# Kernel optimization log

Hardware: AMD Instinct MI355X
Metric: run time of the kernel (lower is better)

## Reference

```python
import jax, jax.numpy as jnp
import numpy as np

K, D = 1024, 256


def setup_inputs() -> dict:
    key = jax.random.key(0)
    k1, k2 = jax.random.split(key)
    z_e = jax.random.normal(k1, (32, D, 32, 32), dtype=jnp.float32)
    # torch init: uniform_(-1/K, 1/K)
    emb_weight = jax.random.uniform(k2, (K, D), minval=-1.0 / K, maxval=1.0 / K, dtype=jnp.float32)
    return {"z_e": z_e, "emb_weight": emb_weight}


def reference(z_e, emb_weight):
    B, C, W, H = z_e.shape
    # [B, W, H, C] -> flatten to [N, C]
    z = jnp.transpose(z_e, (0, 2, 3, 1))
    z_flat = z.reshape(-1, C)
    # squared euclidean distances; argmin is identical to argmin of cdist
    d2 = (
        jnp.sum(z_flat * z_flat, axis=1, keepdims=True)
        - 2.0 * (z_flat @ emb_weight.T)
        + jnp.sum(emb_weight * emb_weight, axis=1)
    )  # [N, K]
    indices = jnp.argmin(d2, axis=1)  # [N]
    z_q = emb_weight[indices].reshape(B, W, H, C)
    # straight-through: forward value equals z_q, gradient passes to z_e
    z_q_st = z + jax.lax.stop_gradient(z_q - z)
    z_q_out = jnp.transpose(z_q, (0, 3, 1, 2))
    z_q_st_out = jnp.transpose(z_q_st, (0, 3, 1, 2))
    return (z_q_st_out, z_q_out, indices.reshape(B, W * H))
```

## Files before the change

### kernel.cpp

```cpp
#include <hip/hip_runtime.h>
#include <cfloat>
#include <cstdint>

#define THRESH 1.25e-4f

typedef __attribute__((ext_vector_type(8))) _Float16 half8;
typedef __attribute__((ext_vector_type(8))) unsigned short upk8;
typedef __attribute__((ext_vector_type(4))) float facc4;

__device__ __forceinline__ unsigned short f2h(float x) {
  _Float16 h = (_Float16)x;
  return __builtin_bit_cast(unsigned short, h);
}


__global__ __launch_bounds__(256) void precompute_kernel(
    const float* __restrict__ emb, float* __restrict__ Csq,
    unsigned short* __restrict__ ehT, int* __restrict__ flagCount) {
  int blk = blockIdx.x, t = threadIdx.x;
  if (blk < 4) {
    int k = blk * 256 + t;
    const float4* e4 = (const float4*)(emb + ((size_t)k << 8));
    double acc = 0.0;
    for (int d4 = 0; d4 < 64; ++d4) {
      float4 e = e4[d4];
      acc += (double)(e.x * e.x) + (double)(e.y * e.y) +
             (double)(e.z * e.z) + (double)(e.w * e.w);
    }
    Csq[k] = (float)acc;
    if (blk == 0 && t == 0) *flagCount = 0;
  } else {
    int linear = (blk - 4) * 256 + t;
    int code = linear & 1023, kg = linear >> 10;
    const float* ep = emb + ((size_t)code << 8) + (kg << 3);
    float4 e0 = *(const float4*)ep;
    float4 e1 = *(const float4*)(ep + 4);
    upk8 pk;
    pk[0] = f2h(e0.x); pk[1] = f2h(e0.y); pk[2] = f2h(e0.z); pk[3] = f2h(e0.w);
    pk[4] = f2h(e1.x); pk[5] = f2h(e1.y); pk[6] = f2h(e1.z); pk[7] = f2h(e1.w);
    *(upk8*)(ehT + ((size_t)linear << 3)) = pk;
  }
}

__device__ __forceinline__ void stage_half(
    const unsigned short* __restrict__ ehT, char* buf, int h, int t) {
  int w6 = t & 0x1C0;
#pragma unroll
  for (int i = 0; i < 8; ++i) {
    int slot = (i << 9) + t;
    int kg = slot >> 7, cl = slot & 127;
    const unsigned short* g = ehT + (((size_t)(kg << 10) + (h << 7) + cl) << 3);
    char* lp = buf + (((i << 9) + w6) << 4);
    __builtin_amdgcn_global_load_lds(
        (const __attribute__((address_space(1))) unsigned int*)g,
        (__attribute__((address_space(3))) unsigned int*)lp, 16, 0, 0);
  }
}

__global__ __launch_bounds__(512) __attribute__((amdgpu_waves_per_eu(2, 2)))
void phase1_kernel(
    const float* __restrict__ z, const unsigned short* __restrict__ ehT,
    const float* __restrict__ Csq, float* __restrict__ A,
    int* __restrict__ idxbuf, int* __restrict__ flagCount,
    int* __restrict__ flagList) {
  __shared__ char bufA[65536] __attribute__((aligned(16)));
  __shared__ char bufB[65536] __attribute__((aligned(16)));
  __shared__ float Cs[1024];
  __shared__ float mm1[2][4][32], mm2[2][4][32];
  __shared__ int mbi[2][4][32];

  int t = threadIdx.x;
  int n0 = blockIdx.x << 7;
  int b = n0 >> 10, wh0 = n0 & 1023;
  int w = t >> 6, l = t & 63;
  int wv = w & 3, wn = w >> 2;
  int lx = l & 15, lg = l >> 4;

  stage_half(ehT, bufA, 0, t);
  stage_half(ehT, bufB, 1, t);
  ((float2*)Cs)[t] = ((const float2*)Csq)[t];

  half8 afr[2][8];
  double nacc[2] = {0.0, 0.0};
  const float* zb = z + (((size_t)(b * 256)) << 10) + wh0 + wv * 32 + lx;
#pragma unroll
  for (int mi = 0; mi < 2; ++mi) {
#pragma unroll
    for (int kk = 0; kk < 8; ++kk) {
      upk8 pk;
#pragma unroll
      for (int j = 0; j < 8; ++j) {
        int c = kk * 32 + lg * 8 + j;
        float x = zb[((size_t)c << 10) + mi * 16];
        nacc[mi] += (double)(x * x);
        pk[j] = f2h(-2.0f * x);
      }
      afr[mi][kk] = __builtin_bit_cast(half8, pk);
    }
  }
#pragma unroll
  for (int mi = 0; mi < 2; ++mi) {
    double s = nacc[mi];
    s += __shfl_xor(s, 16);
    s += __shfl_xor(s, 32);
    if (wn == 0 && lg == 0) A[n0 + wv * 32 + mi * 16 + lx] = (float)s;
  }
  __syncthreads();

  float m1[8], m2[8];
  int bi[8];
#pragma unroll
  for (int s8 = 0; s8 < 8; ++s8) { m1[s8] = FLT_MAX; m2[s8] = FLT_MAX; bi[s8] = 0; }

#pragma unroll 1
  for (int h = 0; h < 8; ++h) {
    const char* buf = (h & 1) ? bufB : bufA;
    facc4 acc[2][4];
#pragma unroll
    for (int mi = 0; mi < 2; ++mi)
#pragma unroll
      for (int nj = 0; nj < 4; ++nj) {
        facc4 zf = {0.0f, 0.0f, 0.0f, 0.0f};
        acc[mi][nj] = zf;
      }
#pragma unroll
    for (int kk = 0; kk < 8; ++kk) {
      const char* base = buf + (((((kk << 2) + lg) << 7) + (wn << 6) + lx) << 4);
#pragma unroll
      for (int nj = 0; nj < 4; ++nj) {
        half8 bv = *(const half8*)(base + (nj << 8));
        acc[0][nj] = __builtin_amdgcn_mfma_f32_16x16x32_f16(afr[0][kk], bv, acc[0][nj], 0, 0, 0);
        acc[1][nj] = __builtin_amdgcn_mfma_f32_16x16x32_f16(afr[1][kk], bv, acc[1][nj], 0, 0, 0);
      }
    }
    int cbase = (h << 7) + (wn << 6);
#pragma unroll
    for (int nj = 0; nj < 4; ++nj) {
      float csv = Cs[cbase + nj * 16 + lx];
      int code = cbase + nj * 16 + lx;
#pragma unroll
      for (int mi = 0; mi < 2; ++mi)
#pragma unroll
        for (int reg = 0; reg < 4; ++reg) {
          int s8 = mi * 4 + reg;
          float sv = acc[mi][nj][reg] + csv;
          float hi = fmaxf(sv, m1[s8]);
          bool lt = sv < m1[s8];
          m1[s8] = lt ? sv : m1[s8];
          bi[s8] = lt ? code : bi[s8];
          m2[s8] = fminf(m2[s8], hi);
        }
    }
    if (h < 7) {
      asm volatile("s_waitcnt lgkmcnt(0)" ::: "memory");
      __builtin_amdgcn_s_barrier();
      if (h < 6) {
        stage_half(ehT, (h & 1) ? bufB : bufA, h + 2, t);
        asm volatile("s_waitcnt vmcnt(8)" ::: "memory");
      } else {
        asm volatile("s_waitcnt vmcnt(0)" ::: "memory");
      }
      __builtin_amdgcn_s_barrier();
    }
  }

#pragma unroll
  for (int s8 = 0; s8 < 8; ++s8) {
    float M1 = m1[s8], M2 = m2[s8];
    int BI = bi[s8];
    for (int off = 8; off > 0; off >>= 1) {
      float om1 = __shfl_xor(M1, off, 16);
      float om2 = __shfl_xor(M2, off, 16);
      int obi = __shfl_xor(BI, off, 16);
      float lo = fminf(M2, om2);
      bool take = (om1 < M1) || (om1 == M1 && obi < BI);
      float loser = take ? M1 : om1;
      M2 = fminf(lo, loser);
      if (take) { M1 = om1; BI = obi; }
    }
    if (lx == 0) {
      int row = ((s8 >> 2) << 4) + (lg << 2) + (s8 & 3);
      mm1[wn][wv][row] = M1; mm2[wn][wv][row] = M2; mbi[wn][wv][row] = BI;
    }
  }
  __syncthreads();
  if (wn == 0 && lx == 0) {
#pragma unroll
    for (int s8 = 0; s8 < 8; ++s8) {
      int row = ((s8 >> 2) << 4) + (lg << 2) + (s8 & 3);
      float a1v = mm1[0][wv][row], a2v = mm2[0][wv][row];
      int ab = mbi[0][wv][row];
      float b1v = mm1[1][wv][row], b2v = mm2[1][wv][row];
      int bb = mbi[1][wv][row];
      bool tb = (b1v < a1v) || (b1v == a1v && bb < ab);
      float M1 = tb ? b1v : a1v;
      int BI = tb ? bb : ab;
      float M2 = fminf(fminf(a2v, b2v), tb ? a1v : b1v);
      int n = n0 + wv * 32 + row;
      idxbuf[n] = BI;
      if (M2 - M1 < THRESH) {
        int pos = atomicAdd(flagCount, 1);
        flagList[pos] = n;
      }
    }
  }
}

__global__ __launch_bounds__(256) void phase2_kernel(
    const float* __restrict__ z, const float* __restrict__ emb,
    const float* __restrict__ Csq, const float* __restrict__ A,
    int* __restrict__ idxbuf, const int* __restrict__ flagCount,
    const int* __restrict__ flagList) {
  __shared__ float zq[4][260];
  __shared__ float Anv[4];
  __shared__ int nn[4];
  __shared__ float sq[4][4];
  __shared__ int sk[4][4];
  int t = threadIdx.x;
  int w = t >> 6, l = t & 63;
  int cnt = *flagCount;
  int nit = (cnt + 3) >> 2;
  for (int it = blockIdx.x; it < nit; it += gridDim.x) {
    __syncthreads();
    int base = it << 2;
    int mcnt = min(4, cnt - base);
    if (t < 4) {
      if (t < mcnt) { int n = flagList[base + t]; nn[t] = n; Anv[t] = A[n]; }
      else nn[t] = -1;
    }
    __syncthreads();
#pragma unroll
    for (int v = 0; v < 4; ++v) {
      int n = nn[v];
      if (n >= 0) {
        int bb = n >> 10, wh = n & 1023;
        zq[v][t] = z[(((size_t)(bb * 256 + t)) << 10) + wh];
      }
    }
    __syncthreads();

    float dot[4][4];
#pragma unroll
    for (int r = 0; r < 4; ++r)
#pragma unroll
      for (int v = 0; v < 4; ++v) dot[r][v] = 0.0f;

    const float4* e0 = (const float4*)(emb + ((size_t)(t + 0) << 8));
    const float4* e1 = (const float4*)(emb + ((size_t)(t + 256) << 8));
    const float4* e2 = (const float4*)(emb + ((size_t)(t + 512) << 8));
    const float4* e3 = (const float4*)(emb + ((size_t)(t + 768) << 8));
#pragma unroll 8
    for (int d4 = 0; d4 < 64; ++d4) {
      float4 ea = e0[d4], eb = e1[d4], ec = e2[d4], ed = e3[d4];
#pragma unroll
      for (int v = 0; v < 4; ++v) {
        float4 zv = *(const float4*)&zq[v][d4 * 4];
        dot[0][v] += zv.x * ea.x + zv.y * ea.y + zv.z * ea.z + zv.w * ea.w;
        dot[1][v] += zv.x * eb.x + zv.y * eb.y + zv.z * eb.z + zv.w * eb.w;
        dot[2][v] += zv.x * ec.x + zv.y * ec.y + zv.z * ec.z + zv.w * ec.w;
        dot[3][v] += zv.x * ed.x + zv.y * ed.y + zv.z * ed.z + zv.w * ed.w;
      }
    }

    float bq[4];
    int bk[4];
#pragma unroll
    for (int v = 0; v < 4; ++v) { bq[v] = FLT_MAX; bk[v] = 0; }
#pragma unroll
    for (int r = 0; r < 4; ++r) {
      int k = t + (r << 8);
      float Ck = Csq[k];
#pragma unroll
      for (int v = 0; v < 4; ++v) {
        float qv = (Anv[v] - 2.0f * dot[r][v]) + Ck;
        if (qv < bq[v]) { bq[v] = qv; bk[v] = k; }
      }
    }

#pragma unroll
    for (int v = 0; v < 4; ++v) {
      float q = bq[v];
      int kk = bk[v];
      for (int off = 32; off > 0; off >>= 1) {
        float oq = __shfl_xor(q, off);
        int ok = __shfl_xor(kk, off);
        if (oq < q || (oq == q && ok < kk)) { q = oq; kk = ok; }
      }
      if (l == 0) { sq[v][w] = q; sk[v][w] = kk; }
    }
    __syncthreads();
    if (t < mcnt) {
      float q = sq[t][0];
      int kk = sk[t][0];
#pragma unroll
      for (int j = 1; j < 4; ++j) {
        float oq = sq[t][j];
        int ok = sk[t][j];
        if (oq < q || (oq == q && ok < kk)) { q = oq; kk = ok; }
      }
      idxbuf[nn[t]] = kk;
    }
  }
}

__global__ __launch_bounds__(256) void gather_kernel(
    const float* __restrict__ emb, const int* __restrict__ idxbuf,
    float* __restrict__ out) {
  __shared__ int sidx[32];
  __shared__ float se[256][34];
  int tid = threadIdx.x;
  int blk = blockIdx.x;
  int n0 = blk * 32;
  int b = n0 >> 10, wh0 = n0 & 1023;
  float* out0 = out;
  float* out1 = out + 8388608;
  float* out2 = out + 16777216;
  if (tid < 32) {
    int ix = idxbuf[n0 + tid];
    sidx[tid] = ix;
    out2[n0 + tid] = (float)ix;
  }
  __syncthreads();
  {
    int v = tid >> 3, d8 = tid & 7;
    int row = sidx[v];
    const float4* e4 = (const float4*)(emb + ((size_t)row << 8));
    for (int it = 0; it < 8; ++it) {
      int d4 = it * 8 + d8;
      float4 e = e4[d4];
      se[d4 * 4 + 0][v] = e.x; se[d4 * 4 + 1][v] = e.y;
      se[d4 * 4 + 2][v] = e.z; se[d4 * 4 + 3][v] = e.w;
    }
  }
  __syncthreads();
  {
    int v = tid & 31, cg = tid >> 5;
    for (int c = cg; c < 256; c += 8) {
      float val = se[c][v];
      size_t o = (((size_t)(b * 256 + c)) << 10) + wh0 + v;
      out0[o] = val;
      out1[o] = val;
    }
  }
}

extern "C" void kernel_launch(void* const* d_in, const int* in_sizes, int n_in,
                              void* d_out, int out_size, void* d_ws, size_t ws_size,
                              hipStream_t stream) {
  const float* z = (const float*)d_in[0];
  const float* emb = (const float*)d_in[1];
  float* ws = (float*)d_ws;
  float* Csq = ws;
  float* A = ws + 1024;
  int* idxbuf = (int*)(ws + 33792);
  int* flagCount = (int*)(ws + 66560);
  int* flagList = (int*)(ws + 66576);
  unsigned short* ehT = (unsigned short*)(ws + 99344);

  precompute_kernel<<<132, 256, 0, stream>>>(emb, Csq, ehT, flagCount);
  phase1_kernel<<<256, 512, 0, stream>>>(z, ehT, Csq, A, idxbuf, flagCount, flagList);
  phase2_kernel<<<1024, 256, 0, stream>>>(z, emb, Csq, A, idxbuf, flagCount, flagList);
  gather_kernel<<<1024, 256, 0, stream>>>(emb, idxbuf, (float*)d_out);
}
```

Baseline: 101.9 us.

## Stage z tile through LDS for coalesced loads and vectorize gather stores

New measurement: 112.2 us. 1.1x slower.

```diff
diff --git a/kernel.cpp b/kernel.cpp
--- a/kernel.cpp
+++ b/kernel.cpp
@@ -76,28 +76,43 @@
   int wv = w & 3, wn = w >> 2;
   int lx = l & 15, lg = l >> 4;
 
-  stage_half(ehT, bufA, 0, t);
-  stage_half(ehT, bufB, 1, t);
+  stage_half(ehT, bufB, 0, t);
   ((float2*)Cs)[t] = ((const float2*)Csq)[t];
 
+  float* zraw = (float*)bufA;
   half8 afr[2][8];
   double nacc[2] = {0.0, 0.0};
-  const float* zb = z + (((size_t)(b * 256)) << 10) + wh0 + wv * 32 + lx;
-#pragma unroll
-  for (int mi = 0; mi < 2; ++mi) {
-#pragma unroll
-    for (int kk = 0; kk < 8; ++kk) {
-      upk8 pk;
-#pragma unroll
-      for (int j = 0; j < 8; ++j) {
-        int c = kk * 32 + lg * 8 + j;
-        float x = zb[((size_t)c << 10) + mi * 16];
-        nacc[mi] += (double)(x * x);
-        pk[j] = f2h(-2.0f * x);
-      }
-      afr[mi][kk] = __builtin_bit_cast(half8, pk);
-    }
-  }
+  int vld = t & 127, rgrp = t >> 7;
+  const float* zbase = z + (((size_t)(b * 256)) << 10) + wh0;
+#pragma unroll 1
+  for (int cq = 0; cq < 4; ++cq) {
+    __syncthreads();
+#pragma unroll
+    for (int r = 0; r < 16; ++r) {
+      int cl = rgrp * 16 + r;
+      zraw[cl * 130 + vld] = zbase[(((size_t)(cq * 64 + cl)) << 10) + vld];
+    }
+    __syncthreads();
+#pragma unroll
+    for (int kh = 0; kh < 2; ++kh) {
+      int kk = cq * 2 + kh;
+#pragma unroll
+      for (int mi = 0; mi < 2; ++mi) {
+        upk8 pk;
+#pragma unroll
+        for (int j = 0; j < 8; ++j) {
+          float x = zraw[(kh * 32 + lg * 8 + j) * 130 + wv * 32 + mi * 16 + lx];
+          nacc[mi] += (double)(x * x);
+          pk[j] = f2h(-2.0f * x);
+        }
+        afr[mi][kk] = __builtin_bit_cast(half8, pk);
+      }
+    }
+  }
+  asm volatile("s_waitcnt lgkmcnt(0)" ::: "memory");
+  __builtin_amdgcn_s_barrier();
+  stage_half(ehT, bufA, 1, t);
+
 #pragma unroll
   for (int mi = 0; mi < 2; ++mi) {
     double s = nacc[mi];
@@ -105,7 +120,8 @@
     s += __shfl_xor(s, 32);
     if (wn == 0 && lg == 0) A[n0 + wv * 32 + mi * 16 + lx] = (float)s;
   }
-  __syncthreads();
+  asm volatile("s_waitcnt vmcnt(0) lgkmcnt(0)" ::: "memory");
+  __builtin_amdgcn_s_barrier();
 
   float m1[8], m2[8];
   int bi[8];
@@ -114,7 +130,7 @@
 
 #pragma unroll 1
   for (int h = 0; h < 8; ++h) {
-    const char* buf = (h & 1) ? bufB : bufA;
+    const char* buf = (h & 1) ? bufA : bufB;
     facc4 acc[2][4];
 #pragma unroll
     for (int mi = 0; mi < 2; ++mi)
@@ -155,7 +171,7 @@
       asm volatile("s_waitcnt lgkmcnt(0)" ::: "memory");
       __builtin_amdgcn_s_barrier();
       if (h < 6) {
-        stage_half(ehT, (h & 1) ? bufB : bufA, h + 2, t);
+        stage_half(ehT, (h & 1) ? bufA : bufB, h + 2, t);
         asm volatile("s_waitcnt vmcnt(8)" ::: "memory");
       } else {
         asm volatile("s_waitcnt vmcnt(0)" ::: "memory");
@@ -307,7 +323,7 @@
     const float* __restrict__ emb, const int* __restrict__ idxbuf,
     float* __restrict__ out) {
   __shared__ int sidx[32];
-  __shared__ float se[256][34];
+  __shared__ float se[256][36];
   int tid = threadIdx.x;
   int blk = blockIdx.x;
   int n0 = blk * 32;
@@ -334,12 +350,14 @@
   }
   __syncthreads();
   {
-    int v = tid & 31, cg = tid >> 5;
-    for (int c = cg; c < 256; c += 8) {
-      float val = se[c][v];
-      size_t o = (((size_t)(b * 256 + c)) << 10) + wh0 + v;
-      out0[o] = val;
-      out1[o] = val;
+    int slot = tid & 7, crow = tid >> 3;
+#pragma unroll
+    for (int it = 0; it < 8; ++it) {
+      int c = it * 32 + crow;
+      float4 val = *(const float4*)&se[c][slot * 4];
+      size_t o = (((size_t)(b * 256 + c)) << 10) + wh0 + slot * 4;
+      *(float4*)(out0 + o) = val;
+      *(float4*)(out1 + o) = val;
     }
   }
 }
```

## Split codebook across two blocks per row tile and merge partial argmins

Applied to the files above, without the earlier changes.

Result: slower. 119.5 us (+17.3%).

```diff
diff --git a/kernel.cpp b/kernel.cpp
--- a/kernel.cpp
+++ b/kernel.cpp
@@ -42,14 +42,14 @@
   }
 }
 
-__device__ __forceinline__ void stage_half(
-    const unsigned short* __restrict__ ehT, char* buf, int h, int t) {
+__device__ __forceinline__ void stage_q(
+    const unsigned short* __restrict__ ehT, char* buf, int gq, int t) {
   int w6 = t & 0x1C0;
 #pragma unroll
-  for (int i = 0; i < 8; ++i) {
+  for (int i = 0; i < 4; ++i) {
     int slot = (i << 9) + t;
-    int kg = slot >> 7, cl = slot & 127;
-    const unsigned short* g = ehT + (((size_t)(kg << 10) + (h << 7) + cl) << 3);
+    int kg = slot >> 6, cl = slot & 63;
+    const unsigned short* g = ehT + (((size_t)(kg << 10) + (gq << 6) + cl) << 3);
     char* lp = buf + (((i << 9) + w6) << 4);
     __builtin_amdgcn_global_load_lds(
         (const __attribute__((address_space(1))) unsigned int*)g,
@@ -57,27 +57,28 @@
   }
 }
 
-__global__ __launch_bounds__(512) __attribute__((amdgpu_waves_per_eu(2, 2)))
-void phase1_kernel(
+__global__ __launch_bounds__(512, 4) void phase1_kernel(
     const float* __restrict__ z, const unsigned short* __restrict__ ehT,
     const float* __restrict__ Csq, float* __restrict__ A,
-    int* __restrict__ idxbuf, int* __restrict__ flagCount,
-    int* __restrict__ flagList) {
-  __shared__ char bufA[65536] __attribute__((aligned(16)));
-  __shared__ char bufB[65536] __attribute__((aligned(16)));
+    float* __restrict__ pm1, float* __restrict__ pm2, int* __restrict__ pbi) {
+  __shared__ char bufA[32768] __attribute__((aligned(16)));
+  __shared__ char bufB[32768] __attribute__((aligned(16)));
   __shared__ float Cs[1024];
   __shared__ float mm1[2][4][32], mm2[2][4][32];
   __shared__ int mbi[2][4][32];
 
   int t = threadIdx.x;
-  int n0 = blockIdx.x << 7;
+  int bid = blockIdx.x;
+  int mtile = bid >> 1, ntile = bid & 1;
+  int n0 = mtile << 7;
+  int c0 = ntile << 9;
   int b = n0 >> 10, wh0 = n0 & 1023;
   int w = t >> 6, l = t & 63;
   int wv = w & 3, wn = w >> 2;
   int lx = l & 15, lg = l >> 4;
 
-  stage_half(ehT, bufA, 0, t);
-  stage_half(ehT, bufB, 1, t);
+  stage_q(ehT, bufA, ntile * 8 + 0, t);
+  stage_q(ehT, bufB, ntile * 8 + 1, t);
   ((float2*)Cs)[t] = ((const float2*)Csq)[t];
 
   half8 afr[2][8];
@@ -98,14 +99,17 @@
       afr[mi][kk] = __builtin_bit_cast(half8, pk);
     }
   }
-#pragma unroll
-  for (int mi = 0; mi < 2; ++mi) {
-    double s = nacc[mi];
-    s += __shfl_xor(s, 16);
-    s += __shfl_xor(s, 32);
-    if (wn == 0 && lg == 0) A[n0 + wv * 32 + mi * 16 + lx] = (float)s;
-  }
-  __syncthreads();
+  if (ntile == 0) {
+#pragma unroll
+    for (int mi = 0; mi < 2; ++mi) {
+      double s = nacc[mi];
+      s += __shfl_xor(s, 16);
+      s += __shfl_xor(s, 32);
+      if (wn == 0 && lg == 0) A[n0 + wv * 32 + mi * 16 + lx] = (float)s;
+    }
+  }
+  asm volatile("s_waitcnt vmcnt(0) lgkmcnt(0)" ::: "memory");
+  __builtin_amdgcn_s_barrier();
 
   float m1[8], m2[8];
   int bi[8];
@@ -113,29 +117,29 @@
   for (int s8 = 0; s8 < 8; ++s8) { m1[s8] = FLT_MAX; m2[s8] = FLT_MAX; bi[s8] = 0; }
 
 #pragma unroll 1
-  for (int h = 0; h < 8; ++h) {
-    const char* buf = (h & 1) ? bufB : bufA;
-    facc4 acc[2][4];
+  for (int q = 0; q < 8; ++q) {
+    const char* buf = (q & 1) ? bufB : bufA;
+    facc4 acc[2][2];
 #pragma unroll
     for (int mi = 0; mi < 2; ++mi)
 #pragma unroll
-      for (int nj = 0; nj < 4; ++nj) {
+      for (int nj = 0; nj < 2; ++nj) {
         facc4 zf = {0.0f, 0.0f, 0.0f, 0.0f};
         acc[mi][nj] = zf;
       }
 #pragma unroll
     for (int kk = 0; kk < 8; ++kk) {
-      const char* base = buf + (((((kk << 2) + lg) << 7) + (wn << 6) + lx) << 4);
-#pragma unroll
-      for (int nj = 0; nj < 4; ++nj) {
+      const char* base = buf + (((((kk << 2) + lg) << 6) + (wn << 5) + lx) << 4);
+#pragma unroll
+      for (int nj = 0; nj < 2; ++nj) {
         half8 bv = *(const half8*)(base + (nj << 8));
         acc[0][nj] = __builtin_amdgcn_mfma_f32_16x16x32_f16(afr[0][kk], bv, acc[0][nj], 0, 0, 0);
         acc[1][nj] = __builtin_amdgcn_mfma_f32_16x16x32_f16(afr[1][kk], bv, acc[1][nj], 0, 0, 0);
       }
     }
-    int cbase = (h << 7) + (wn << 6);
-#pragma unroll
-    for (int nj = 0; nj < 4; ++nj) {
+    int cbase = c0 + (q << 6) + (wn << 5);
+#pragma unroll
+    for (int nj = 0; nj < 2; ++nj) {
       float csv = Cs[cbase + nj * 16 + lx];
       int code = cbase + nj * 16 + lx;
 #pragma unroll
@@ -151,12 +155,12 @@
           m2[s8] = fminf(m2[s8], hi);
         }
     }
-    if (h < 7) {
+    if (q < 7) {
       asm volatile("s_waitcnt lgkmcnt(0)" ::: "memory");
       __builtin_amdgcn_s_barrier();
-      if (h < 6) {
-        stage_half(ehT, (h & 1) ? bufB : bufA, h + 2, t);
-        asm volatile("s_waitcnt vmcnt(8)" ::: "memory");
+      if (q < 6) {
+        stage_q(ehT, (q & 1) ? bufB : bufA, ntile * 8 + q + 2, t);
+        asm volatile("s_waitcnt vmcnt(4)" ::: "memory");
       } else {
         asm volatile("s_waitcnt vmcnt(0)" ::: "memory");
       }
@@ -197,12 +201,29 @@
       int BI = tb ? bb : ab;
       float M2 = fminf(fminf(a2v, b2v), tb ? a1v : b1v);
       int n = n0 + wv * 32 + row;
-      idxbuf[n] = BI;
-      if (M2 - M1 < THRESH) {
-        int pos = atomicAdd(flagCount, 1);
-        flagList[pos] = n;
-      }
-    }
+      size_t o = ((size_t)ntile << 15) + n;
+      pm1[o] = M1; pm2[o] = M2; pbi[o] = BI;
+    }
+  }
+}
+
+__global__ __launch_bounds__(256) void merge_kernel(
+    const float* __restrict__ pm1, const float* __restrict__ pm2,
+    const int* __restrict__ pbi, int* __restrict__ idxbuf,
+    int* __restrict__ flagCount, int* __restrict__ flagList) {
+  int n = blockIdx.x * 256 + threadIdx.x;
+  float M1 = pm1[n], M2 = pm2[n];
+  int BI = pbi[n];
+  float b1 = pm1[32768 + n], b2 = pm2[32768 + n];
+  int bb = pbi[32768 + n];
+  bool tb = (b1 < M1) || (b1 == M1 && bb < BI);
+  float loser = tb ? M1 : b1;
+  M2 = fminf(fminf(M2, b2), loser);
+  if (tb) { M1 = b1; BI = bb; }
+  idxbuf[n] = BI;
+  if (M2 - M1 < THRESH) {
+    int pos = atomicAdd(flagCount, 1);
+    flagList[pos] = n;
   }
 }
 
@@ -357,8 +378,13 @@
   int* flagList = (int*)(ws + 66576);
   unsigned short* ehT = (unsigned short*)(ws + 99344);
 
+  float* pm1 = (float*)d_out;
+  float* pm2 = pm1 + 65536;
+  int* pbi = (int*)(pm2 + 65536);
+
   precompute_kernel<<<132, 256, 0, stream>>>(emb, Csq, ehT, flagCount);
-  phase1_kernel<<<256, 512, 0, stream>>>(z, ehT, Csq, A, idxbuf, flagCount, flagList);
+  phase1_kernel<<<512, 512, 0, stream>>>(z, ehT, Csq, A, pm1, pm2, pbi);
+  merge_kernel<<<128, 256, 0, stream>>>(pm1, pm2, pbi, idxbuf, flagCount, flagList);
   phase2_kernel<<<1024, 256, 0, stream>>>(z, emb, Csq, A, idxbuf, flagCount, flagList);
   gather_kernel<<<1024, 256, 0, stream>>>(emb, idxbuf, (float*)d_out);
 }
```
